# Performance work log

Hardware: AMD Instinct MI355X
Metric: run time of the kernel (lower is better)

Reference implementation:

```python
import jax, jax.numpy as jnp
import numpy as np

T = 16          # time_span
N = 128         # num_trajectory
D = 512         # embedding dim
TEMP = 0.1      # temperature
INF = 1000000000.0
M = 2 * N * T   # total rows of z (two views)


def setup_inputs() -> dict:
    key = jax.random.key(0)
    k1, k2 = jax.random.split(key)
    z = jax.random.normal(k1, (M, D), dtype=jnp.float32)
    done = jax.random.randint(k2, (T, N), 0, 2).astype(jnp.int32)  # [T, N] binary done flags
    return {"z": z, "done": done}


def _build_positive_mask(done):
    # done: [T, N] int -> transposed to [N, T] as in the torch code
    d = done.astype(jnp.float32).T  # [N, T]
    # Sequential rewrite loop is equivalent to:
    #   done_new[r,t] = 1 iff exists original done at p < t in row r AND orig done[r,t] == 0
    excl = jnp.cumsum(d, axis=1) - d  # exclusive cumsum along time
    d_new = jnp.where((excl > 0) & (d == 0), 1.0, 0.0)  # [N, T]
    done_vec = 1.0 - d_new.reshape(-1)  # [N*T]
    # block-diagonal temporal mask: same trajectory => 1
    traj = jnp.arange(N * T) // T
    block = (traj[:, None] == traj[None, :]).astype(jnp.float32)  # [NT, NT]
    done_mask = (done_vec[:, None] * done_vec[None, :]) * block
    done_mask = jnp.tile(done_mask, (2, 2))      # [M, M]
    temporal_mask = jnp.tile(block, (2, 2))      # [M, M]
    eye = jnp.eye(M, dtype=jnp.float32)
    positive_mask = (1.0 - done_mask) * (1.0 - temporal_mask) + eye
    return positive_mask, eye


def reference(z, done):
    positive_mask, eye = _build_positive_mask(done)
    # cosine similarity = normalize + GEMM (same math as broadcasted F.cosine_similarity)
    norms = jnp.maximum(jnp.linalg.norm(z, axis=-1, keepdims=True), 1e-8)
    zn = z / norms
    logits = (zn @ zn.T) / TEMP - eye * INF  # [M, M]
    log_probs = jax.nn.log_softmax(logits, axis=1)
    neg = 1.0 - positive_mask
    mean_log_prob = jnp.sum(neg * log_probs, axis=1) / jnp.sum(neg, axis=1)
    return -jnp.mean(mean_log_prob)
```

## Files before the change

### kernel.cpp

```cpp
#include <hip/hip_runtime.h>
#include <hip/hip_bf16.h>

typedef float f32x16 __attribute__((ext_vector_type(16)));
typedef unsigned short u16;
typedef unsigned char u8;
typedef unsigned int u32;
typedef unsigned long long u64;
typedef u32 u32x4 __attribute__((ext_vector_type(4)));
typedef u64 u64x2 __attribute__((ext_vector_type(2)));


__device__ inline void async_cp16(const u8* g, u8* l) {
    __builtin_amdgcn_global_load_lds(
        (const __attribute__((address_space(1))) unsigned int*)g,
        (__attribute__((address_space(3))) unsigned int*)l, 16, 0, 0);
}

__global__ void nrm_kernel(const float* __restrict__ z, u8* __restrict__ zn8,
                           float* __restrict__ expsum, float* __restrict__ possum) {
    int row = blockIdx.x;
    int tid = threadIdx.x;
    float4 v = ((const float4*)(z + row * 512))[tid];
    float ss = v.x * v.x + v.y * v.y + v.z * v.z + v.w * v.w;
#pragma unroll
    for (int off = 32; off; off >>= 1) ss += __shfl_down(ss, off, 64);
    __shared__ float red[2];
    if ((tid & 63) == 0) red[tid >> 6] = ss;
    __syncthreads();
    float sc = 1.0f / fmaxf(sqrtf(red[0] + red[1]), 1e-8f);
    u32 w = __builtin_amdgcn_cvt_pk_fp8_f32(v.x * sc, v.y * sc, 0, false);
    w = __builtin_amdgcn_cvt_pk_fp8_f32(v.z * sc, v.w * sc, w, true);
    ((u32*)(zn8 + (size_t)row * 512))[tid] = w;
    if (tid == 0) { expsum[row] = 0.f; possum[row] = 0.f; }
}

__global__ void pos_kernel(const u8* __restrict__ zn8, float* __restrict__ possum) {
    int g = blockIdx.x;
    int l = threadIdx.x;
    int u = l & 31, h = l >> 5;
    int grow = (u < 16) ? (g * 16 + u) : (2048 + g * 16 + (u - 16));
    const u64* src = (const u64*)(zn8 + (size_t)grow * 512);
    f32x16 acc = {};
#pragma unroll
    for (int kc = 0; kc < 32; ++kc) {
        u64 f = src[2 * kc + h];
        acc = __builtin_amdgcn_mfma_f32_32x32x16_fp8_fp8((long)f, (long)f, acc, 0, 0, 0);
    }
#pragma unroll
    for (int r = 0; r < 16; ++r) {
        int rrow = (r & 3) + 8 * (r >> 2) + 4 * h;
        float v = (rrow == u) ? 0.f : acc[r];
        v += __shfl_xor(v, 1, 64);
        v += __shfl_xor(v, 2, 64);
        v += __shfl_xor(v, 4, 64);
        v += __shfl_xor(v, 8, 64);
        v += __shfl_xor(v, 16, 64);
        if (u == 0) {
            int gr = (rrow < 16) ? (g * 16 + rrow) : (2048 + g * 16 + (rrow - 16));
            possum[gr] = v * 10.0f;
        }
    }
}

__global__ __launch_bounds__(256, 2) void gemm_kernel(const u8* __restrict__ zn8,
                                                      float* __restrict__ expsum) {
    __shared__ u8 Bt[2][32 * 512];
    int wave = threadIdx.x >> 6;
    int l = threadIdx.x & 63;
    int m = l & 31, h = l >> 5;

    int t = blockIdx.x, i = 0;
    while (t >= 32 - i) { t -= 32 - i; ++i; }
    int j = i + t;
    int rowbase = i * 128 + wave * 32;
    bool diagwg = (i == j);

    long af[32];
    {
        const u32x4* arow = (const u32x4*)(zn8 + (size_t)(rowbase + m) * 512);
#pragma unroll
        for (int p = 0; p < 2; ++p) {
            u32x4 t16[16];
#pragma unroll
            for (int g2 = 0; g2 < 16; ++g2) t16[g2] = arow[p * 16 + g2];
#pragma unroll
            for (int g2 = 0; g2 < 16; ++g2) {
                u64x2 q = __builtin_bit_cast(u64x2, t16[g2]);
                af[p * 16 + g2] = (long)(h ? q.y : q.x);
            }
        }
    }

    float expacc[16];
#pragma unroll
    for (int r = 0; r < 16; ++r) expacc[r] = 0.f;

    auto stage = [&](int buf, int ct) {
        int colbase = j * 128 + ct * 32;
#pragma unroll
        for (int it = 0; it < 4; ++it) {
            int c = wave * 8 + 2 * it;
            int C = colbase + c + h;
            int srcoff = (m ^ (C & 7)) * 16;
            async_cp16(zn8 + (size_t)C * 512 + srcoff, &Bt[buf][c * 512]);
        }
    };

    stage(0, 0);
    int sB16 = (m & 7) * 16;
    for (int ct = 0; ct < 4; ++ct) {
        __syncthreads();
        if (ct < 3) stage((ct + 1) & 1, ct + 1);
        const u8* bcol = &Bt[ct & 1][m * 512 + h * 8];
        f32x16 acc = {};
#pragma unroll
        for (int kc = 0; kc < 32; ++kc) {
            u64 bf = *(const u64*)(bcol + ((kc * 16) ^ sB16));
            acc = __builtin_amdgcn_mfma_f32_32x32x16_fp8_fp8(af[kc], (long)bf, acc, 0, 0, 0);
        }
        int colbase = j * 128 + ct * 32;
        bool diagtile = diagwg && (ct == wave);
        float cs = 0.f;
#pragma unroll
        for (int r = 0; r < 16; ++r) {
            int rrow = (r & 3) + 8 * (r >> 2) + 4 * h;
            float e = (diagtile && rrow == m) ? 0.f : __expf(acc[r] * 10.0f);
            expacc[r] += e;
            cs += e;
        }
        if (!diagwg) {
            cs += __shfl_xor(cs, 32, 64);
            if (h == 0) atomicAdd(&expsum[colbase + m], cs);
        }
    }
#pragma unroll
    for (int r = 0; r < 16; ++r) {
        float v = expacc[r];
        v += __shfl_xor(v, 1, 64);
        v += __shfl_xor(v, 2, 64);
        v += __shfl_xor(v, 4, 64);
        v += __shfl_xor(v, 8, 64);
        v += __shfl_xor(v, 16, 64);
        if (m == 0) {
            int rrow = (r & 3) + 8 * (r >> 2) + 4 * h;
            atomicAdd(&expsum[rowbase + rrow], v);
        }
    }
}

__global__ void fin_kernel(const float* __restrict__ expsum,
                           const float* __restrict__ possum, float* __restrict__ out) {
    int tid = threadIdx.x;
    float s = 0.f;
    for (int i = tid; i < 4096; i += 1024)
        s += __logf(expsum[i]) - possum[i] * (1.0f / 31.0f);
#pragma unroll
    for (int off = 32; off; off >>= 1) s += __shfl_down(s, off, 64);
    __shared__ float red[16];
    if ((tid & 63) == 0) red[tid >> 6] = s;
    __syncthreads();
    if (tid == 0) {
        float tt = 0.f;
#pragma unroll
        for (int i2 = 0; i2 < 16; ++i2) tt += red[i2];
        out[0] = tt * (1.0f / 4096.0f);
    }
}

extern "C" void kernel_launch(void* const* d_in, const int* in_sizes, int n_in,
                              void* d_out, int out_size, void* d_ws, size_t ws_size,
                              hipStream_t stream) {
    const float* z = (const float*)d_in[0];
    u8* zn8 = (u8*)d_ws;
    float* expsum = (float*)((char*)d_ws + (2u << 20));
    float* possum = expsum + 4096;
    float* out = (float*)d_out;

    nrm_kernel<<<4096, 128, 0, stream>>>(z, zn8, expsum, possum);
    pos_kernel<<<128, 64, 0, stream>>>(zn8, possum);
    gemm_kernel<<<528, 256, 0, stream>>>(zn8, expsum);
    fin_kernel<<<1, 1024, 0, stream>>>(expsum, possum, out);
}
```

Baseline: 99.86 us.

## Replace global atomics with per-tile partial sums reduced in final kernel

Each GEMM workgroup now reduces its row and column exp-sums in shared memory and writes them to a dense partial buffer indexed by tile pair, instead of doing many global atomicAdds into expsum. The final kernel sums the 32 partials per row before taking the log, so the zero-init in the normalization kernel is removed. The A-fragment load is simplified to direct 8-byte loads, and launch bounds go from 2 to 3 blocks per CU. The cost is extra global traffic (about 0.5 MB of partials) and a heavier single-block final reduction.

```diff
diff --git a/kernel.cpp b/kernel.cpp
--- a/kernel.cpp
+++ b/kernel.cpp
@@ -6,8 +6,6 @@
 typedef unsigned char u8;
 typedef unsigned int u32;
 typedef unsigned long long u64;
-typedef u32 u32x4 __attribute__((ext_vector_type(4)));
-typedef u64 u64x2 __attribute__((ext_vector_type(2)));
 
 
 __device__ inline void async_cp16(const u8* g, u8* l) {
@@ -16,8 +14,7 @@
         (__attribute__((address_space(3))) unsigned int*)l, 16, 0, 0);
 }
 
-__global__ void nrm_kernel(const float* __restrict__ z, u8* __restrict__ zn8,
-                           float* __restrict__ expsum, float* __restrict__ possum) {
+__global__ void nrm_kernel(const float* __restrict__ z, u8* __restrict__ zn8) {
     int row = blockIdx.x;
     int tid = threadIdx.x;
     float4 v = ((const float4*)(z + row * 512))[tid];
@@ -31,7 +28,6 @@
     u32 w = __builtin_amdgcn_cvt_pk_fp8_f32(v.x * sc, v.y * sc, 0, false);
     w = __builtin_amdgcn_cvt_pk_fp8_f32(v.z * sc, v.w * sc, w, true);
     ((u32*)(zn8 + (size_t)row * 512))[tid] = w;
-    if (tid == 0) { expsum[row] = 0.f; possum[row] = 0.f; }
 }
 
 __global__ void pos_kernel(const u8* __restrict__ zn8, float* __restrict__ possum) {
@@ -62,9 +58,11 @@
     }
 }
 
-__global__ __launch_bounds__(256, 2) void gemm_kernel(const u8* __restrict__ zn8,
-                                                      float* __restrict__ expsum) {
+__global__ __launch_bounds__(256, 3) void gemm_kernel(const u8* __restrict__ zn8,
+                                                      float* __restrict__ part) {
     __shared__ u8 Bt[2][32 * 512];
+    __shared__ float colred[4][4][32];
+    __shared__ float rowred[128];
     int wave = threadIdx.x >> 6;
     int l = threadIdx.x & 63;
     int m = l & 31, h = l >> 5;
@@ -77,18 +75,9 @@
 
     long af[32];
     {
-        const u32x4* arow = (const u32x4*)(zn8 + (size_t)(rowbase + m) * 512);
+        const u8* arow = zn8 + (size_t)(rowbase + m) * 512 + h * 8;
 #pragma unroll
-        for (int p = 0; p < 2; ++p) {
-            u32x4 t16[16];
-#pragma unroll
-            for (int g2 = 0; g2 < 16; ++g2) t16[g2] = arow[p * 16 + g2];
-#pragma unroll
-            for (int g2 = 0; g2 < 16; ++g2) {
-                u64x2 q = __builtin_bit_cast(u64x2, t16[g2]);
-                af[p * 16 + g2] = (long)(h ? q.y : q.x);
-            }
-        }
+        for (int kc = 0; kc < 32; ++kc) af[kc] = *(const long*)(arow + kc * 16);
     }
 
     float expacc[16];
@@ -118,7 +107,6 @@
             u64 bf = *(const u64*)(bcol + ((kc * 16) ^ sB16));
             acc = __builtin_amdgcn_mfma_f32_32x32x16_fp8_fp8(af[kc], (long)bf, acc, 0, 0, 0);
         }
-        int colbase = j * 128 + ct * 32;
         bool diagtile = diagwg && (ct == wave);
         float cs = 0.f;
 #pragma unroll
@@ -128,11 +116,10 @@
             expacc[r] += e;
             cs += e;
         }
-        if (!diagwg) {
-            cs += __shfl_xor(cs, 32, 64);
-            if (h == 0) atomicAdd(&expsum[colbase + m], cs);
-        }
+        cs += __shfl_xor(cs, 32, 64);
+        if (h == 0) colred[wave][ct][m] = cs;
     }
+
 #pragma unroll
     for (int r = 0; r < 16; ++r) {
         float v = expacc[r];
@@ -143,17 +130,33 @@
         v += __shfl_xor(v, 16, 64);
         if (m == 0) {
             int rrow = (r & 3) + 8 * (r >> 2) + 4 * h;
-            atomicAdd(&expsum[rowbase + rrow], v);
+            rowred[wave * 32 + rrow] = v;
+        }
+    }
+    __syncthreads();
+    if (threadIdx.x < 128) {
+        int tid = threadIdx.x;
+        part[(size_t)(i * 32 + j) * 128 + tid] = rowred[tid];
+        if (!diagwg) {
+            int tt = tid >> 5, c2 = tid & 31;
+            float cv = colred[0][tt][c2] + colred[1][tt][c2] +
+                       colred[2][tt][c2] + colred[3][tt][c2];
+            part[(size_t)(j * 32 + i) * 128 + tid] = cv;
         }
     }
 }
 
-__global__ void fin_kernel(const float* __restrict__ expsum,
+__global__ void fin_kernel(const float* __restrict__ part,
                            const float* __restrict__ possum, float* __restrict__ out) {
     int tid = threadIdx.x;
     float s = 0.f;
-    for (int i = tid; i < 4096; i += 1024)
-        s += __logf(expsum[i]) - possum[i] * (1.0f / 31.0f);
+    for (int r = tid; r < 4096; r += 1024) {
+        int b = r >> 7, rr = r & 127;
+        float es = 0.f;
+#pragma unroll
+        for (int sl = 0; sl < 32; ++sl) es += part[(size_t)(b * 32 + sl) * 128 + rr];
+        s += __logf(es) - possum[r] * (1.0f / 31.0f);
+    }
 #pragma unroll
     for (int off = 32; off; off >>= 1) s += __shfl_down(s, off, 64);
     __shared__ float red[16];
@@ -172,12 +175,12 @@
                               hipStream_t stream) {
     const float* z = (const float*)d_in[0];
     u8* zn8 = (u8*)d_ws;
-    float* expsum = (float*)((char*)d_ws + (2u << 20));
-    float* possum = expsum + 4096;
+    float* part = (float*)((char*)d_ws + (2u << 20));
+    float* possum = part + 32 * 32 * 128;
     float* out = (float*)d_out;
 
-    nrm_kernel<<<4096, 128, 0, stream>>>(z, zn8, expsum, possum);
+    nrm_kernel<<<4096, 128, 0, stream>>>(z, zn8);
     pos_kernel<<<128, 64, 0, stream>>>(zn8, possum);
-    gemm_kernel<<<528, 256, 0, stream>>>(zn8, expsum);
-    fin_kernel<<<1, 1024, 0, stream>>>(expsum, possum, out);
+    gemm_kernel<<<528, 256, 0, stream>>>(zn8, part);
+    fin_kernel<<<1, 1024, 0, stream>>>(part, possum, out);
 }
```

Result: no change. 99.40 us (-0.5%).
